# Performance work log

Measured on AMD Instinct MI355X. Metric: run time of the kernel, lower is better.

The kernel has to match this reference:

```python
import jax, jax.numpy as jnp
import numpy as np

EPS = 1e-5

def _ln(x, g=None, b=None):
    m = x.mean(-1, keepdims=True)
    v = x.var(-1, keepdims=True)
    y = (x - m) / jnp.sqrt(v + EPS)
    if g is not None:
        y = y * g + b
    return y

def setup_inputs() -> dict:
    B, N, D, E, NC = 32, 256, 1024, 4096, 16
    key = jax.random.key(0)
    ks = iter(jax.random.split(key, 24))
    def rn(shape, s=0.02):
        return jax.random.normal(next(ks), shape, jnp.float32) * s
    return dict(
        h=jax.random.normal(next(ks), (B, N, D), jnp.float32),
        Wpp=rn((D, E)), bpp=jnp.zeros(E), Wsp=rn((D, E)), bsp=jnp.zeros(E),
        Wq=rn((E, E)), bq=jnp.zeros(E),
        Wk=rn((E, E)), bk=jnp.zeros(E),
        Wv=rn((E, E)), bv=jnp.zeros(E),
        g_pfs=jnp.ones(D + E), b_pfs=jnp.zeros(D + E),
        Wpfs=rn((D + E, D)), bpfs=jnp.zeros(D),
        g_sfs=jnp.ones(E), b_sfs=jnp.zeros(E),
        Wsfs=rn((E, D)), bsfs=jnp.zeros(D),
        Wpc=rn((D, NC)), bpc=jnp.zeros(NC),
        Wc0=rn((NC, 8, D)), bc0=jnp.zeros((NC, 8)),
        Wc1=rn((NC, 16, D)), bc1=jnp.zeros((NC, 16)),
        Wc2=rn((NC, 32, D)), bc2=jnp.zeros((NC, 32)),
    )

def reference(h, Wpp, bpp, Wsp, bsp, Wq, bq, Wk, bk, Wv, bv,
              g_pfs, b_pfs, Wpfs, bpfs, g_sfs, b_sfs, Wsfs, bsfs,
              Wpc, bpc, Wc0, bc0, Wc1, bc1, Wc2, bc2):
    B, N, D = h.shape
    H = 4
    E = Wpp.shape[1]
    hd = E // H
    scale = hd ** -0.5
    gelu = lambda x: jax.nn.gelu(x, approximate=False)  # torch exact GELU
    pp = gelu(h @ Wpp + bpp)                  # [B,N,E]
    sp = gelu(h @ Wsp + bsp)                  # [B,N,E]
    Q = (pp @ Wq + bq).reshape(B, N, H, hd)
    K = (sp @ Wk + bk).reshape(B, N, H, hd)
    V = (sp @ Wv + bv).reshape(B, N, H, hd)
    attn = jax.nn.softmax(jnp.einsum('bqhd,bkhd->bhqk', Q, K) * scale, axis=-1)
    intf = jnp.einsum('bhqk,bkhd->bqhd', attn, V).reshape(B, N, E)
    intf = _ln(intf)                          # F.layer_norm, no affine
    pvec = _ln((_ln(jnp.concatenate([h, intf], -1), g_pfs, b_pfs) @ Wpfs + bpfs).mean(1))  # [B,D]
    svec = _ln((_ln(sp, g_sfs, b_sfs) @ Wsfs + bsfs).mean(1))                               # [B,D]
    parent_logits = pvec @ Wpc + bpc          # [B,NC]
    y_hat = jnp.argmax(parent_logits, axis=1) # argmax(softmax) == argmax(logits)
    # routed child heads: gather per-sample weight by parent argmax, batched matvec
    child = tuple(
        jnp.einsum('bd,bnd->bn', svec, W[y_hat]) + b[y_hat]
        for W, b in ((Wc0, bc0), (Wc1, bc1), (Wc2, bc2))
    )
    return (parent_logits,) + child + (pvec, svec)
```

## Files before the change

### kernel.cpp

```cpp
#include <hip/hip_runtime.h>
#include <hip/hip_bf16.h>

typedef __bf16 bf16x8 __attribute__((ext_vector_type(8)));
typedef float f32x4 __attribute__((ext_vector_type(4)));
typedef unsigned long long u64;

#define EPSV 1e-5f

__device__ __forceinline__ float bf2f(unsigned short u){
  unsigned int x = ((unsigned int)u) << 16;
  return __builtin_bit_cast(float, x);
}
__device__ __forceinline__ unsigned short f2bf(float f){
  __bf16 b = (__bf16)f;
  return __builtin_bit_cast(unsigned short, b);
}
__device__ __forceinline__ float gelu_exact(float x){
  return 0.5f * x * (1.0f + erff(x * 0.7071067811865476f));
}
__device__ __forceinline__ void gload_lds16(const void* g, void* l){
  __builtin_amdgcn_global_load_lds((const __attribute__((address_space(1))) unsigned int*)g,
                                   (__attribute__((address_space(3))) unsigned int*)l, 16, 0, 0);
}

template<int MODE>
__global__ __launch_bounds__(512, 2)
void gemm256(const unsigned short* __restrict__ A, const unsigned short* __restrict__ B,
             const float* __restrict__ bias0, const float* __restrict__ bias1,
             void* __restrict__ C0v, void* __restrict__ C1v,
             int Kd, int lda, int ldb, int ldc)
{
  __shared__ char smem[131072];
  const int t = threadIdx.x;
  const int w = t >> 6, l = t & 63;
  const int wm = w >> 2, wn = w & 3;
  const int lr = l & 15, lg = l >> 4;
  const int nbx = gridDim.x;
  const int nwg = nbx * gridDim.y;
  int bid = blockIdx.y*nbx + blockIdx.x;
  if ((nwg & 7) == 0) bid = (bid & 7)*(nwg >> 3) + (bid >> 3);
  const int bm0 = (bid / nbx) * 256, bn0 = (bid % nbx) * 256;
  const int nk = Kd >> 6;

  const int srow = t >> 3;
  const int sslot = t & 7;

  f32x4 acc[8][4];
  #pragma unroll
  for (int i=0;i<8;++i){
    #pragma unroll
    for (int j=0;j<4;++j){ f32x4 zz = {0.f,0.f,0.f,0.f}; acc[i][j] = zz; }
  }
  bf16x8 a0[4][2], a1[4][2], b0[2][2], b1[2][2];

  auto stage = [&](int kt, int mat, int hf, int q){
    if (kt >= nk) return;
    const int r_h = q*64 + srow;
    const int s_ = sslot ^ ((r_h >> 1) & 7);
    const unsigned short* gp = (mat ? B + (size_t)(bn0 + hf*128 + r_h)*ldb
                                    : A + (size_t)(bm0 + hf*128 + r_h)*lda)
                               + (kt << 6) + s_*8;
    char* lp = smem + mat*65536 + (kt&1)*32768 + hf*16384 + q*8192 + t*16;
    gload_lds16((const void*)gp, (void*)lp);
  };
  auto rdA = [&](int d, int fm, int kk)->bf16x8{
    const int r = fm*16 + lr;
    const int s_ = (kk*4 + lg) ^ ((r >> 1) & 7);
    return *(const bf16x8*)(smem + d*32768 + wm*16384 + r*128 + s_*16);
  };
  auto rdB = [&](int d, int fn, int kk)->bf16x8{
    const int r = (wn&1)*64 + fn*16 + lr;
    const int s_ = (kk*4 + lg) ^ ((r >> 1) & 7);
    return *(const bf16x8*)(smem + 65536 + d*32768 + (wn>>1)*16384 + r*128 + s_*16);
  };

  auto ktile = [&](int kt, int d){
    #pragma unroll
    for (int fm=0; fm<4; ++fm){ a0[fm][0] = rdA(d, fm, 0); a0[fm][1] = rdA(d, fm, 1); }
    #pragma unroll
    for (int fn=0; fn<2; ++fn){ b0[fn][0] = rdB(d, fn, 0); b0[fn][1] = rdB(d, fn, 1); }
    stage(kt+1, 0, 0, 1); stage(kt+1, 0, 1, 1);
    __builtin_amdgcn_s_barrier();
    __builtin_amdgcn_sched_barrier(0);
    __builtin_amdgcn_s_setprio(1);
    #pragma unroll
    for (int fm=0; fm<4; ++fm)
      #pragma unroll
      for (int fn=0; fn<2; ++fn)
        #pragma unroll
        for (int kk=0; kk<2; ++kk)
          acc[fm][fn] = __builtin_amdgcn_mfma_f32_16x16x32_bf16(a0[fm][kk], b0[fn][kk], acc[fm][fn], 0,0,0);
    __builtin_amdgcn_s_setprio(0);
    __builtin_amdgcn_s_barrier();
    #pragma unroll
    for (int fn=0; fn<2; ++fn){ b1[fn][0] = rdB(d, fn+2, 0); b1[fn][1] = rdB(d, fn+2, 1); }
    stage(kt+2, 0, 0, 0); stage(kt+2, 0, 1, 0);
    __builtin_amdgcn_s_barrier();
    __builtin_amdgcn_sched_barrier(0);
    __builtin_amdgcn_s_setprio(1);
    #pragma unroll
    for (int fm=0; fm<4; ++fm)
      #pragma unroll
      for (int fn=0; fn<2; ++fn)
        #pragma unroll
        for (int kk=0; kk<2; ++kk)
          acc[fm][fn+2] = __builtin_amdgcn_mfma_f32_16x16x32_bf16(a0[fm][kk], b1[fn][kk], acc[fm][fn+2], 0,0,0);
    __builtin_amdgcn_s_setprio(0);
    __builtin_amdgcn_s_barrier();
    #pragma unroll
    for (int fm=0; fm<4; ++fm){ a1[fm][0] = rdA(d, fm+4, 0); a1[fm][1] = rdA(d, fm+4, 1); }
    stage(kt+2, 1, 0, 0); stage(kt+2, 1, 1, 0);
    __builtin_amdgcn_s_barrier();
    __builtin_amdgcn_sched_barrier(0);
    __builtin_amdgcn_s_setprio(1);
    #pragma unroll
    for (int fm=0; fm<4; ++fm)
      #pragma unroll
      for (int fn=0; fn<2; ++fn)
        #pragma unroll
        for (int kk=0; kk<2; ++kk)
          acc[fm+4][fn+2] = __builtin_amdgcn_mfma_f32_16x16x32_bf16(a1[fm][kk], b1[fn][kk], acc[fm+4][fn+2], 0,0,0);
    __builtin_amdgcn_s_setprio(0);
    __builtin_amdgcn_s_barrier();
    stage(kt+2, 1, 0, 1); stage(kt+2, 1, 1, 1);
    __builtin_amdgcn_s_setprio(1);
    #pragma unroll
    for (int fm=0; fm<4; ++fm)
      #pragma unroll
      for (int fn=0; fn<2; ++fn)
        #pragma unroll
        for (int kk=0; kk<2; ++kk)
          acc[fm+4][fn] = __builtin_amdgcn_mfma_f32_16x16x32_bf16(a1[fm][kk], b0[fn][kk], acc[fm+4][fn], 0,0,0);
    __builtin_amdgcn_s_setprio(0);
    if (kt + 2 < nk) { asm volatile("s_waitcnt vmcnt(6)" ::: "memory"); }
    else             { asm volatile("s_waitcnt vmcnt(0)" ::: "memory"); }
    __builtin_amdgcn_s_barrier();
  };

  stage(0,0,0,0); stage(0,0,1,0); stage(0,0,0,1); stage(0,0,1,1);
  stage(0,1,0,0); stage(0,1,1,0); stage(0,1,0,1); stage(0,1,1,1);
  stage(1,0,0,0); stage(1,0,1,0);
  stage(1,1,0,0); stage(1,1,1,0); stage(1,1,0,1); stage(1,1,1,1);
  asm volatile("s_waitcnt vmcnt(6)" ::: "memory");
  __builtin_amdgcn_s_barrier();

  for (int kt = 0; kt < nk; kt += 2){ ktile(kt, 0); ktile(kt+1, 1); }

  #pragma unroll
  for (int fm=0; fm<8; ++fm){
    #pragma unroll
    for (int fn=0; fn<4; ++fn){
      const int row0 = bm0 + wm*128 + fm*16 + lg*4;
      const int col  = bn0 + wn*64 + fn*16 + lr;
      f32x4 v = acc[fm][fn];
      if constexpr (MODE == 3){
        unsigned short* C = (unsigned short*)C0v;
        const float bb = bias0[col];
        u64 pack = 0;
        #pragma unroll
        for (int j=0;j<4;++j) pack |= (u64)f2bf(v[j] + bb) << (16*j);
        *(u64*)(C + (size_t)col*256 + (size_t)(row0>>8)*1048576 + (row0&255)) = pack;
      } else if constexpr (MODE == 4){
        if (col < 4096){
          unsigned short* C = (unsigned short*)C0v;
          const float bb = bias0[col];
          #pragma unroll
          for (int j=0;j<4;++j) C[(size_t)(row0+j)*ldc + col] = f2bf(v[j] + bb);
        } else {
          const int c2 = col - 4096;
          unsigned short* C = (unsigned short*)C1v;
          const float bb = bias1[c2];
          u64 pack = 0;
          #pragma unroll
          for (int j=0;j<4;++j) pack |= (u64)f2bf(v[j] + bb) << (16*j);
          *(u64*)(C + (size_t)c2*256 + (size_t)(row0>>8)*1048576 + (row0&255)) = pack;
        }
      } else {
        const bool hi = (MODE == 0) && (col >= 4096);
        unsigned short* C = (unsigned short*)(hi ? C1v : C0v);
        const int c2 = hi ? (col - 4096) : col;
        const float bb = hi ? bias1[c2] : bias0[c2];
        #pragma unroll
        for (int j=0;j<4;++j){
          float x = v[j] + bb;
          if constexpr (MODE==0) x = gelu_exact(x);
          C[(size_t)(row0+j)*ldc + c2] = f2bf(x);
        }
      }
    }
  }
}

template<int MODE>
__global__ __launch_bounds__(256)
void gemm_bt(const unsigned short* __restrict__ A, const unsigned short* __restrict__ B,
             const float* __restrict__ bias, void* __restrict__ Cv,
             int Kd, int lda, int ldb, int ldc,
             long sA2, long sA1, long sB2, long sB1, long sC2, long sC1,
             float scale)
{
  __shared__ unsigned short lds[2][2][4096];
  const int t = threadIdx.x;
  const int w = t >> 6, l = t & 63;
  const int z = blockIdx.z;
  A += (size_t)(z>>2)*sA2 + (size_t)(z&3)*sA1;
  B += (size_t)(z>>2)*sB2 + (size_t)(z&3)*sB1;
  const int bm0 = blockIdx.y * 128, bn0 = blockIdx.x * 128;
  const int nk = Kd >> 5;

  const int sr = l >> 2;
  const int ss = l & 3;

  f32x4 acc[4][4];
  #pragma unroll
  for (int i=0;i<4;++i){
    #pragma unroll
    for (int j=0;j<4;++j){ f32x4 zz = {0.f,0.f,0.f,0.f}; acc[i][j] = zz; }
  }

  const int wm = w >> 1, wn = w & 1;
  const int lr = l & 15, lg = l >> 4;

  auto stage = [&](int kt, int bb){
    const int k0 = kt << 5;
    #pragma unroll
    for (int i=0;i<2;++i){
      const int r  = w*32 + i*16 + sr;
      const int sa = ss ^ ((r>>1)&3);
      const unsigned short* ga = A + (size_t)(bm0 + r)*lda + (k0 + sa*8);
      gload_lds16((const void*)ga, (void*)((char*)&lds[bb][0][0] + w*2048 + i*1024));
      const unsigned short* gb = B + (size_t)(bn0 + r)*ldb + (k0 + sa*8);
      gload_lds16((const void*)gb, (void*)((char*)&lds[bb][1][0] + w*2048 + i*1024));
    }
  };

  int buf = 0;
  stage(0, 0);
  for (int kt=0; kt<nk; ++kt){
    __syncthreads();
    if (kt+1 < nk) stage(kt+1, buf^1);
    bf16x8 av[4], bv[4];
    #pragma unroll
    for (int fm=0; fm<4; ++fm){
      const int row = wm*64 + fm*16 + lr;
      const int sl  = lg ^ ((row>>1)&3);
      av[fm] = *(const bf16x8*)((const char*)&lds[buf][0][0] + row*64 + sl*16);
    }
    #pragma unroll
    for (int fn=0; fn<4; ++fn){
      const int col = wn*64 + fn*16 + lr;
      const int sl  = lg ^ ((col>>1)&3);
      bv[fn] = *(const bf16x8*)((const char*)&lds[buf][1][0] + col*64 + sl*16);
    }
    #pragma unroll
    for (int fm=0; fm<4; ++fm){
      #pragma unroll
      for (int fn=0; fn<4; ++fn)
        acc[fm][fn] = __builtin_amdgcn_mfma_f32_16x16x32_bf16(av[fm], bv[fn], acc[fm][fn], 0,0,0);
    }
    buf ^= 1;
  }

  const size_t coff = (size_t)(z>>2)*sC2 + (size_t)(z&3)*sC1;
  #pragma unroll
  for (int fm=0; fm<4; ++fm){
    #pragma unroll
    for (int fn=0; fn<4; ++fn){
      const int row0 = bm0 + wm*64 + fm*16 + lg*4;
      const int col  = bn0 + wn*64 + fn*16 + lr;
      f32x4 v = acc[fm][fn];
      if constexpr (MODE == 2){
        float* C = (float*)Cv + coff;
        #pragma unroll
        for (int j=0;j<4;++j) C[(size_t)(row0+j)*ldc + col] = v[j]*scale;
      }
    }
  }
}

__global__ __launch_bounds__(256)
void k_convh(const float* __restrict__ in, unsigned short* __restrict__ out){
  const size_t id = (size_t)blockIdx.x*256 + threadIdx.x;
  float4 v = ((const float4*)in)[id];
  u64 pack = (u64)f2bf(v.x) | ((u64)f2bf(v.y)<<16) | ((u64)f2bf(v.z)<<32) | ((u64)f2bf(v.w)<<48);
  *(u64*)(out + id*4) = pack;
}

__global__ __launch_bounds__(256)
void k_tconv(const float* __restrict__ W, unsigned short* __restrict__ Wt, int Kd, int N){
  __shared__ float lt[64][65];
  const int t = threadIdx.x;
  const int n0 = blockIdx.x*64, k0 = blockIdx.y*64;
  #pragma unroll
  for (int i=0;i<16;++i){
    int lin = i*256 + t; int r = lin>>6, c = lin&63;
    lt[r][c] = W[(size_t)(k0+r)*N + n0 + c];
  }
  __syncthreads();
  #pragma unroll
  for (int i=0;i<16;++i){
    int lin = i*256 + t; int n = lin>>6, k = lin&63;
    Wt[(size_t)(n0+n)*Kd + k0 + k] = f2bf(lt[k][n]);
  }
}

__global__ __launch_bounds__(256)
void k_softmax(const float* __restrict__ S, unsigned short* __restrict__ P){
  const int t = threadIdx.x, w = t>>6, l = t&63;
  const size_t row = (size_t)blockIdx.x*4 + w;
  float4 v = *(const float4*)(S + row*256 + l*4);
  float m = fmaxf(fmaxf(v.x,v.y), fmaxf(v.z,v.w));
  #pragma unroll
  for (int off=32; off; off>>=1) m = fmaxf(m, __shfl_xor(m, off));
  float e0 = expf(v.x-m), e1 = expf(v.y-m), e2 = expf(v.z-m), e3 = expf(v.w-m);
  float s = e0+e1+e2+e3;
  #pragma unroll
  for (int off=32; off; off>>=1) s += __shfl_xor(s, off);
  const float inv = 1.0f/s;
  u64 pack = (u64)f2bf(e0*inv) | ((u64)f2bf(e1*inv)<<16) | ((u64)f2bf(e2*inv)<<32) | ((u64)f2bf(e3*inv)<<48);
  *(u64*)(P + row*256 + l*4) = pack;
}

__device__ __forceinline__ void blkred2(float& a, float& b, float* sred, int t){
  #pragma unroll
  for (int off=32; off; off>>=1){ a += __shfl_xor(a, off); b += __shfl_xor(b, off); }
  __syncthreads();
  if ((t&63)==0){ sred[(t>>6)*2] = a; sred[(t>>6)*2+1] = b; }
  __syncthreads();
  a = sred[0]+sred[2]+sred[4]+sred[6];
  b = sred[1]+sred[3]+sred[5]+sred[7];
}

__global__ __launch_bounds__(256)
void k_stats(const float* __restrict__ h, const float* __restrict__ intf,
             const unsigned short* __restrict__ sp,
             const float* __restrict__ g_pfs, const float* __restrict__ b_pfs,
             const float* __restrict__ g_sfs, const float* __restrict__ b_sfs,
             float* __restrict__ part_p, float* __restrict__ part_s, int g0)
{
  __shared__ float sred[8];
  const int bl = blockIdx.x, grp = blockIdx.y, t = threadIdx.x;
  float zacc[20], wacc[16];
  #pragma unroll
  for (int j=0;j<20;++j) zacc[j]=0.f;
  #pragma unroll
  for (int j=0;j<16;++j) wacc[j]=0.f;
  for (int rr=0; rr<32; ++rr){
    const size_t r = (size_t)bl*256 + grp*32 + rr;
    float hv[4], iv[16], sv[16];
    #pragma unroll
    for (int j=0;j<4;++j) hv[j] = h[r*1024 + j*256 + t];
    float s1=0.f, s2=0.f;
    #pragma unroll
    for (int j=0;j<16;++j){ float x = intf[r*4096 + j*256 + t]; iv[j]=x; s1+=x; s2+=x*x; }
    blkred2(s1,s2,sred,t);
    const float m1 = s1*(1.f/4096.f);
    const float rs1 = rsqrtf(fmaxf(s2*(1.f/4096.f) - m1*m1, 0.f) + EPSV);
    float t1=0.f, t2=0.f;
    #pragma unroll
    for (int j=0;j<4;++j){ t1 += hv[j]; t2 += hv[j]*hv[j]; }
    #pragma unroll
    for (int j=0;j<16;++j){ float y = (iv[j]-m1)*rs1; iv[j]=y; t1+=y; t2+=y*y; }
    blkred2(t1,t2,sred,t);
    const float m2 = t1*(1.f/5120.f);
    const float rs2 = rsqrtf(fmaxf(t2*(1.f/5120.f) - m2*m2, 0.f) + EPSV);
    #pragma unroll
    for (int j=0;j<4;++j){ int idx = j*256+t; zacc[j] += ((hv[j]-m2)*rs2)*g_pfs[idx] + b_pfs[idx]; }
    #pragma unroll
    for (int j=0;j<16;++j){ int idx = 1024 + j*256+t; zacc[4+j] += ((iv[j]-m2)*rs2)*g_pfs[idx] + b_pfs[idx]; }
    float u1=0.f, u2=0.f;
    #pragma unroll
    for (int j=0;j<16;++j){ float x = bf2f(sp[r*4096 + j*256 + t]); sv[j]=x; u1+=x; u2+=x*x; }
    blkred2(u1,u2,sred,t);
    const float m3 = u1*(1.f/4096.f);
    const float rs3 = rsqrtf(fmaxf(u2*(1.f/4096.f) - m3*m3, 0.f) + EPSV);
    #pragma unroll
    for (int j=0;j<16;++j){ int idx = j*256+t; wacc[j] += ((sv[j]-m3)*rs3)*g_sfs[idx] + b_sfs[idx]; }
  }
  const size_t pb = (size_t)(g0 + bl)*8 + grp;
  #pragma unroll
  for (int j=0;j<20;++j) part_p[pb*5120 + j*256 + t] = zacc[j];
  #pragma unroll
  for (int j=0;j<16;++j) part_s[pb*4096 + j*256 + t] = wacc[j];
}

__global__ __launch_bounds__(256)
void k_reduce(const float* __restrict__ part_p, const float* __restrict__ part_s,
              float* __restrict__ xbar, float* __restrict__ ybar){
  int id = blockIdx.x*256 + threadIdx.x;
  if (id < 32*5120){
    const int b = id / 5120, i = id % 5120;
    float s = 0.f;
    for (int g=0; g<8; ++g) s += part_p[((size_t)b*8+g)*5120 + i];
    xbar[(size_t)b*5120 + i] = s * (1.f/256.f);
  } else {
    id -= 32*5120;
    const int b = id / 4096, i = id % 4096;
    float s = 0.f;
    for (int g=0; g<8; ++g) s += part_s[((size_t)b*8+g)*4096 + i];
    ybar[(size_t)b*4096 + i] = s * (1.f/256.f);
  }
}

__global__ __launch_bounds__(256)
void k_proj_part(const float* __restrict__ xbar, const float* __restrict__ ybar,
                 const float* __restrict__ Wpfs, const float* __restrict__ Wsfs,
                 float* __restrict__ pbuf){
  const int path = blockIdx.z;
  const int y = blockIdx.y;
  if (path == 1 && y >= 8) return;
  const int Kp = path ? 4096 : 5120;
  const float* X = path ? ybar : xbar;
  const float* W = path ? Wsfs : Wpfs;
  const int t = threadIdx.x;
  const int col = blockIdx.x*64 + (t & 63);
  const int sub = t >> 6;
  const int k0 = y*512 + sub*128;
  float acc[32];
  #pragma unroll
  for (int b=0;b<32;++b) acc[b] = 0.f;
  for (int i4=0; i4<32; ++i4){
    const int k = k0 + i4*4;
    float wv0 = W[(size_t)(k  )*1024 + col];
    float wv1 = W[(size_t)(k+1)*1024 + col];
    float wv2 = W[(size_t)(k+2)*1024 + col];
    float wv3 = W[(size_t)(k+3)*1024 + col];
    #pragma unroll
    for (int b=0;b<32;++b){
      float4 xv = *(const float4*)(X + (size_t)b*Kp + k);
      acc[b] += xv.x*wv0 + xv.y*wv1 + xv.z*wv2 + xv.w*wv3;
    }
  }
  float* dst = pbuf + ((size_t)(path*40 + y*4 + sub)*32)*1024 + col;
  #pragma unroll
  for (int b=0;b<32;++b) dst[(size_t)b*1024] = acc[b];
}

__global__ __launch_bounds__(256)
void k_projred(const float* __restrict__ pbuf,
               const float* __restrict__ bpfs, const float* __restrict__ bsfs,
               float* __restrict__ tpre, float* __restrict__ spre){
  const int id = blockIdx.x*256 + threadIdx.x;
  const int path = id >> 15;
  const int rem = id & 32767;
  const int b = rem >> 10, col = rem & 1023;
  const int ns = path ? 32 : 40;
  const float* src = pbuf + ((size_t)(path*40)*32 + b)*1024 + col;
  float s = path ? bsfs[col] : bpfs[col];
  for (int g=0; g<ns; ++g) s += src[(size_t)g*32*1024];
  (path ? spre : tpre)[(size_t)b*1024 + col] = s;
}

__global__ __launch_bounds__(256)
void k_lnrow(const float* __restrict__ tpre, const float* __restrict__ spre,
             float* __restrict__ out){
  __shared__ float sred[8];
  const int id = blockIdx.x, t = threadIdx.x;
  const int path = id >> 5, b = id & 31;
  const float* src = (path ? spre : tpre) + (size_t)b*1024;
  float v[4]; float s1=0.f, s2=0.f;
  #pragma unroll
  for (int j=0;j<4;++j){ v[j] = src[j*256+t]; s1 += v[j]; s2 += v[j]*v[j]; }
  blkred2(s1,s2,sred,t);
  const float m = s1*(1.f/1024.f);
  const float rs = rsqrtf(fmaxf(s2*(1.f/1024.f)-m*m,0.f)+EPSV);
  float* dst = out + (path ? 35072 : 2304) + (size_t)b*1024;
  #pragma unroll
  for (int j=0;j<4;++j) dst[j*256+t] = (v[j]-m)*rs;
}

__global__ __launch_bounds__(256)
void k_head(const float* __restrict__ Wpc, const float* __restrict__ bpc,
            const float* __restrict__ Wc0, const float* __restrict__ bc0,
            const float* __restrict__ Wc1, const float* __restrict__ bc1,
            const float* __restrict__ Wc2, const float* __restrict__ bc2,
            float* __restrict__ out){
  __shared__ float slog[16];
  __shared__ int sy;
  const int b = blockIdx.x, t = threadIdx.x, w = t>>6, l = t&63;
  const float* pv = out + 2304 + (size_t)b*1024;
  const float* sv = out + 35072 + (size_t)b*1024;
  #pragma unroll
  for (int jj=0; jj<4; ++jj){
    const int j = w*4 + jj;
    float a = 0.f;
    for (int i=l; i<1024; i+=64) a += pv[i]*Wpc[(size_t)i*16 + j];
    #pragma unroll
    for (int off=32; off; off>>=1) a += __shfl_xor(a, off);
    if (l==0){ const float lgv = a + bpc[j]; slog[j] = lgv; out[b*16 + j] = lgv; }
  }
  __syncthreads();
  if (t==0){
    int best=0; float bvv = slog[0];
    for (int i=1;i<16;++i) if (slog[i] > bvv){ bvv = slog[i]; best = i; }
    sy = best;
  }
  __syncthreads();
  const int y = sy;
  const float* Ws[3] = {Wc0, Wc1, Wc2};
  const float* bs[3] = {bc0, bc1, bc2};
  const int nouts[3] = {8,16,32};
  const int ooff[3]  = {512, 768, 1280};
  for (int hI=0; hI<3; ++hI){
    const int no = nouts[hI];
    for (int n = w; n < no; n += 4){
      const float* wr = Ws[hI] + ((size_t)y*no + n)*1024;
      float a = 0.f;
      for (int i=l; i<1024; i+=64) a += sv[i]*wr[i];
      #pragma unroll
      for (int off=32; off; off>>=1) a += __shfl_xor(a, off);
      if (l==0) out[ooff[hI] + b*no + n] = a + bs[hI][(size_t)y*no + n];
    }
  }
}

extern "C" void kernel_launch(void* const* d_in, const int* in_sizes, int n_in,
                              void* d_out, int out_size, void* d_ws, size_t ws_size,
                              hipStream_t stream)
{
  const float* h    = (const float*)d_in[0];
  const float* Wpp  = (const float*)d_in[1];
  const float* bpp  = (const float*)d_in[2];
  const float* Wsp  = (const float*)d_in[3];
  const float* bsp  = (const float*)d_in[4];
  const float* Wq   = (const float*)d_in[5];
  const float* bq   = (const float*)d_in[6];
  const float* Wk   = (const float*)d_in[7];
  const float* bk   = (const float*)d_in[8];
  const float* Wv   = (const float*)d_in[9];
  const float* bv   = (const float*)d_in[10];
  const float* g_pfs= (const float*)d_in[11];
  const float* b_pfs= (const float*)d_in[12];
  const float* Wpfs = (const float*)d_in[13];
  const float* bpfs = (const float*)d_in[14];
  const float* g_sfs= (const float*)d_in[15];
  const float* b_sfs= (const float*)d_in[16];
  const float* Wsfs = (const float*)d_in[17];
  const float* bsfs = (const float*)d_in[18];
  const float* Wpc  = (const float*)d_in[19];
  const float* bpc  = (const float*)d_in[20];
  const float* Wc0  = (const float*)d_in[21];
  const float* bc0  = (const float*)d_in[22];
  const float* Wc1  = (const float*)d_in[23];
  const float* bc1  = (const float*)d_in[24];
  const float* Wc2  = (const float*)d_in[25];
  const float* bc2  = (const float*)d_in[26];
  float* out = (float*)d_out;
  char* ws = (char*)d_ws;
  (void)in_sizes; (void)n_in; (void)out_size;

  struct PlanT { int G, NS, hoist; };
  const PlanT plans[11] = {
    {32,4096,1},{32,4096,0},{16,4096,1},{16,4096,0},{8,4096,1},{8,4096,0},
    {4,4096,0},{2,4096,0},{1,4096,0},{1,2048,0},{1,1024,0}};
  int G = 0, NS = 0, HOIST = 0;
  size_t oWt=0,oWps=0,oWq=0,oWkv=0;
  size_t oPp=0,oPs=0,oXb=0,oYb=0,oTp=0,oSp=0,oPbf=0,oHb=0,oPb=0,oSb=0,oQ=0,oK=0,oVt=0,oS=0,oP=0;
  for (int pi = 0; pi < 11; ++pi){
    const size_t g = plans[pi].G, ns = plans[pi].NS;
    const int hoist = plans[pi].hoist;
    size_t off = 0;
    auto alloc = [&](size_t bytes){ size_t o = off; off += (bytes + 255) & ~255ULL; return o; };
    size_t wt=0, wps=0, wq=0, wkv=0;
    if (hoist){
      wps = alloc(8192ULL*1024*2);
      wq  = alloc(4096ULL*4096*2);
      wkv = alloc(8192ULL*4096*2);
    } else {
      wt = alloc(ns*4096*2);
    }
    size_t pp_ = alloc(32*8*5120*4);
    size_t ps_ = alloc(32*8*4096*4);
    size_t xb = alloc(32*5120*4);
    size_t yb = alloc(32*4096*4);
    size_t tp = alloc(32*1024*4);
    size_t sp_ = alloc(32*1024*4);
    size_t pbf = alloc(2*40*32*1024*4);
    size_t hb = alloc(g*524288);
    size_t pb = alloc(g*2097152);
    size_t sb = alloc(g*2097152);
    size_t q  = alloc(g*2097152);
    size_t k  = alloc(g*2097152);
    size_t vt = alloc(g*2097152);
    size_t s  = alloc(g*1048576);
    size_t p  = alloc(g*524288);
    if (off <= ws_size){
      G = (int)g; NS = (int)ns; HOIST = hoist;
      oWt=wt; oWps=wps; oWq=wq; oWkv=wkv;
      oPp=pp_; oPs=ps_; oXb=xb; oYb=yb; oTp=tp; oSp=sp_; oPbf=pbf;
      oHb=hb; oPb=pb; oSb=sb; oQ=q; oK=k; oVt=vt; oS=s; oP=p;
      break;
    }
  }
  if (!G) return;

  unsigned short* Wt   = (unsigned short*)(ws + oWt);
  unsigned short* WpsT = (unsigned short*)(ws + oWps);
  unsigned short* WqT  = (unsigned short*)(ws + oWq);
  unsigned short* WkvT = (unsigned short*)(ws + oWkv);
  float* part_p = (float*)(ws + oPp);
  float* part_s = (float*)(ws + oPs);
  float* xbar   = (float*)(ws + oXb);
  float* ybar   = (float*)(ws + oYb);
  float* tpre   = (float*)(ws + oTp);
  float* spre   = (float*)(ws + oSp);
  float* pbuf   = (float*)(ws + oPbf);
  unsigned short* h_bf = (unsigned short*)(ws + oHb);
  unsigned short* pp   = (unsigned short*)(ws + oPb);
  unsigned short* sp   = (unsigned short*)(ws + oSb);
  unsigned short* Q    = (unsigned short*)(ws + oQ);
  unsigned short* Kb   = (unsigned short*)(ws + oK);
  unsigned short* Vt   = (unsigned short*)(ws + oVt);
  float*          S    = (float*)(ws + oS);
  unsigned short* P    = (unsigned short*)(ws + oP);
  float*          intf = (float*)(ws + oQ);

  const float scale = 1.0f/32.0f;
  (void)oK;

  if (HOIST){
    hipLaunchKernelGGL(k_tconv, dim3(64,16), dim3(256), 0, stream, Wpp, WpsT, 1024, 4096);
    hipLaunchKernelGGL(k_tconv, dim3(64,16), dim3(256), 0, stream, Wsp, WpsT + 4096ULL*1024, 1024, 4096);
    hipLaunchKernelGGL(k_tconv, dim3(64,64), dim3(256), 0, stream, Wq, WqT, 4096, 4096);
    hipLaunchKernelGGL(k_tconv, dim3(64,64), dim3(256), 0, stream, Wk, WkvT, 4096, 4096);
    hipLaunchKernelGGL(k_tconv, dim3(64,64), dim3(256), 0, stream, Wv, WkvT + 4096ULL*4096, 4096, 4096);
  }

  for (int g0 = 0; g0 < 32; g0 += G){
    const float* h_g = h + (size_t)g0*262144;

    hipLaunchKernelGGL(k_convh, dim3(G*256), dim3(256), 0, stream, h_g, h_bf);

    if (HOIST){
      hipLaunchKernelGGL(gemm256<0>, dim3(32,G), dim3(512), 0, stream,
                         h_bf, WpsT, bpp, bsp, (void*)pp, (void*)sp, 1024, 1024,1024,4096);
      hipLaunchKernelGGL(gemm256<1>, dim3(16,G), dim3(512), 0, stream,
                         pp, WqT, bq, bq, (void*)Q, (void*)Q, 4096, 4096,4096,4096);
      hipLaunchKernelGGL(gemm256<4>, dim3(32,G), dim3(512), 0, stream,
                         sp, WkvT, bk, bv, (void*)Kb, (void*)Vt, 4096, 4096,4096,4096);
    } else {
      hipLaunchKernelGGL(k_tconv, dim3(64,16), dim3(256), 0, stream, Wpp, Wt, 1024, 4096);
      hipLaunchKernelGGL(gemm256<0>, dim3(16,G), dim3(512), 0, stream,
                         h_bf, Wt, bpp, bpp, (void*)pp, (void*)pp, 1024, 1024,1024,4096);
      for (int nso = 0; nso < 4096; nso += NS){
        hipLaunchKernelGGL(k_tconv, dim3(NS/64,64), dim3(256), 0, stream, Wq + nso, Wt, 4096, 4096);
        hipLaunchKernelGGL(gemm256<1>, dim3(NS/256,G), dim3(512), 0, stream,
                           pp, Wt, bq + nso, bq + nso, (void*)(Q + nso), (void*)(Q + nso), 4096, 4096,4096,4096);
      }
      hipLaunchKernelGGL(k_tconv, dim3(64,16), dim3(256), 0, stream, Wsp, Wt, 1024, 4096);
      hipLaunchKernelGGL(gemm256<0>, dim3(16,G), dim3(512), 0, stream,
                         h_bf, Wt, bsp, bsp, (void*)sp, (void*)sp, 1024, 1024,1024,4096);
      for (int nso = 0; nso < 4096; nso += NS){
        hipLaunchKernelGGL(k_tconv, dim3(NS/64,64), dim3(256), 0, stream, Wk + nso, Wt, 4096, 4096);
        hipLaunchKernelGGL(gemm256<1>, dim3(NS/256,G), dim3(512), 0, stream,
                           sp, Wt, bk + nso, bk + nso, (void*)(Kb + nso), (void*)(Kb + nso), 4096, 4096,4096,4096);
      }
      for (int nso = 0; nso < 4096; nso += NS){
        hipLaunchKernelGGL(k_tconv, dim3(NS/64,64), dim3(256), 0, stream, Wv + nso, Wt, 4096, 4096);
        hipLaunchKernelGGL(gemm256<3>, dim3(NS/256,G), dim3(512), 0, stream,
                           sp, Wt, bv + nso, bv + nso, (void*)(Vt + (size_t)nso*256), (void*)(Vt + (size_t)nso*256), 4096, 4096,4096,256);
      }
    }
    hipLaunchKernelGGL(gemm_bt<2>, dim3(2,2,G*4), dim3(256), 0, stream,
                       Q, Kb, (const float*)nullptr, (void*)S, 1024, 4096,4096,256,
                       1048576L,1024L, 1048576L,1024L, 262144L,65536L, scale);
    hipLaunchKernelGGL(k_softmax, dim3(G*256), dim3(256), 0, stream, S, P);
    hipLaunchKernelGGL(gemm_bt<2>, dim3(8,2,G*4), dim3(256), 0, stream,
                       P, Vt, (const float*)nullptr, (void*)intf, 256, 256,256,4096,
                       262144L,65536L, 1048576L,262144L, 1048576L,1024L, 1.f);
    hipLaunchKernelGGL(k_stats, dim3(G,8), dim3(256), 0, stream,
                       h_g, intf, sp, g_pfs, b_pfs, g_sfs, b_sfs, part_p, part_s, g0);
  }

  hipLaunchKernelGGL(k_reduce, dim3(1152), dim3(256), 0, stream, part_p, part_s, xbar, ybar);
  hipLaunchKernelGGL(k_proj_part, dim3(16,10,2), dim3(256), 0, stream,
                     xbar, ybar, Wpfs, Wsfs, pbuf);
  hipLaunchKernelGGL(k_projred, dim3(256), dim3(256), 0, stream,
                     pbuf, bpfs, bsfs, tpre, spre);
  hipLaunchKernelGGL(k_lnrow, dim3(64), dim3(256), 0, stream, tpre, spre, out);
  hipLaunchKernelGGL(k_head, dim3(32), dim3(256), 0, stream,
                     Wpc, bpc, Wc0, bc0, Wc1, bc1, Wc2, bc2, out);
}
```

Before: 1.518 ms.

## Restructure GEMM k-tile pipeline to prefetch next-tile fragments and finer vmcnt gating

Reorders the four MFMA quadrants per k-tile and moves loading of the a0/b0 register fragments for the next k-tile into the current tile, so the first quadrant of each tile starts without waiting on LDS reads. The staging of global-to-LDS copies is reshuffled and each phase now waits on a vmcnt(4) gate instead of a single vmcnt(6)/0 at the end. The sched_barrier hints are removed. This aims to overlap LDS reads and global loads with MFMA work more evenly. The new vmcnt accounting and staging order must still line up with the buffer reuse, or the kernel can read stale LDS data.

```diff
diff --git a/kernel.cpp b/kernel.cpp
--- a/kernel.cpp
+++ b/kernel.cpp
@@ -22,6 +22,8 @@
   __builtin_amdgcn_global_load_lds((const __attribute__((address_space(1))) unsigned int*)g,
                                    (__attribute__((address_space(3))) unsigned int*)l, 16, 0, 0);
 }
+
+#define VMGATE4() asm volatile("s_waitcnt vmcnt(4)" ::: "memory")
 
 template<int MODE>
 __global__ __launch_bounds__(512, 2)
@@ -76,12 +78,9 @@
 
   auto ktile = [&](int kt, int d){
     #pragma unroll
-    for (int fm=0; fm<4; ++fm){ a0[fm][0] = rdA(d, fm, 0); a0[fm][1] = rdA(d, fm, 1); }
-    #pragma unroll
-    for (int fn=0; fn<2; ++fn){ b0[fn][0] = rdB(d, fn, 0); b0[fn][1] = rdB(d, fn, 1); }
-    stage(kt+1, 0, 0, 1); stage(kt+1, 0, 1, 1);
-    __builtin_amdgcn_s_barrier();
-    __builtin_amdgcn_sched_barrier(0);
+    for (int fm=0; fm<4; ++fm){ a1[fm][0] = rdA(d, fm+4, 0); a1[fm][1] = rdA(d, fm+4, 1); }
+    stage(kt+1, 1, 0, 1); stage(kt+1, 1, 1, 1);
+    __builtin_amdgcn_s_barrier();
     __builtin_amdgcn_s_setprio(1);
     #pragma unroll
     for (int fm=0; fm<4; ++fm)
@@ -91,12 +90,25 @@
         for (int kk=0; kk<2; ++kk)
           acc[fm][fn] = __builtin_amdgcn_mfma_f32_16x16x32_bf16(a0[fm][kk], b0[fn][kk], acc[fm][fn], 0,0,0);
     __builtin_amdgcn_s_setprio(0);
+    VMGATE4();
     __builtin_amdgcn_s_barrier();
     #pragma unroll
     for (int fn=0; fn<2; ++fn){ b1[fn][0] = rdB(d, fn+2, 0); b1[fn][1] = rdB(d, fn+2, 1); }
+    stage(kt+1, 0, 0, 1); stage(kt+1, 0, 1, 1);
+    __builtin_amdgcn_s_barrier();
+    __builtin_amdgcn_s_setprio(1);
+    #pragma unroll
+    for (int fm=0; fm<4; ++fm)
+      #pragma unroll
+      for (int fn=0; fn<2; ++fn)
+        #pragma unroll
+        for (int kk=0; kk<2; ++kk)
+          acc[fm+4][fn] = __builtin_amdgcn_mfma_f32_16x16x32_bf16(a1[fm][kk], b0[fn][kk], acc[fm+4][fn], 0,0,0);
+    __builtin_amdgcn_s_setprio(0);
+    VMGATE4();
+    __builtin_amdgcn_s_barrier();
     stage(kt+2, 0, 0, 0); stage(kt+2, 0, 1, 0);
     __builtin_amdgcn_s_barrier();
-    __builtin_amdgcn_sched_barrier(0);
     __builtin_amdgcn_s_setprio(1);
     #pragma unroll
     for (int fm=0; fm<4; ++fm)
@@ -106,12 +118,16 @@
         for (int kk=0; kk<2; ++kk)
           acc[fm][fn+2] = __builtin_amdgcn_mfma_f32_16x16x32_bf16(a0[fm][kk], b1[fn][kk], acc[fm][fn+2], 0,0,0);
     __builtin_amdgcn_s_setprio(0);
-    __builtin_amdgcn_s_barrier();
-    #pragma unroll
-    for (int fm=0; fm<4; ++fm){ a1[fm][0] = rdA(d, fm+4, 0); a1[fm][1] = rdA(d, fm+4, 1); }
+    VMGATE4();
+    __builtin_amdgcn_s_barrier();
+    if (kt+1 < nk){
+      #pragma unroll
+      for (int fm=0; fm<4; ++fm){ a0[fm][0] = rdA(d^1, fm, 0); a0[fm][1] = rdA(d^1, fm, 1); }
+      #pragma unroll
+      for (int fn=0; fn<2; ++fn){ b0[fn][0] = rdB(d^1, fn, 0); b0[fn][1] = rdB(d^1, fn, 1); }
+    }
     stage(kt+2, 1, 0, 0); stage(kt+2, 1, 1, 0);
     __builtin_amdgcn_s_barrier();
-    __builtin_amdgcn_sched_barrier(0);
     __builtin_amdgcn_s_setprio(1);
     #pragma unroll
     for (int fm=0; fm<4; ++fm)
@@ -121,27 +137,23 @@
         for (int kk=0; kk<2; ++kk)
           acc[fm+4][fn+2] = __builtin_amdgcn_mfma_f32_16x16x32_bf16(a1[fm][kk], b1[fn][kk], acc[fm+4][fn+2], 0,0,0);
     __builtin_amdgcn_s_setprio(0);
-    __builtin_amdgcn_s_barrier();
-    stage(kt+2, 1, 0, 1); stage(kt+2, 1, 1, 1);
-    __builtin_amdgcn_s_setprio(1);
-    #pragma unroll
-    for (int fm=0; fm<4; ++fm)
-      #pragma unroll
-      for (int fn=0; fn<2; ++fn)
-        #pragma unroll
-        for (int kk=0; kk<2; ++kk)
-          acc[fm+4][fn] = __builtin_amdgcn_mfma_f32_16x16x32_bf16(a1[fm][kk], b0[fn][kk], acc[fm+4][fn], 0,0,0);
-    __builtin_amdgcn_s_setprio(0);
-    if (kt + 2 < nk) { asm volatile("s_waitcnt vmcnt(6)" ::: "memory"); }
-    else             { asm volatile("s_waitcnt vmcnt(0)" ::: "memory"); }
+    VMGATE4();
     __builtin_amdgcn_s_barrier();
   };
 
-  stage(0,0,0,0); stage(0,0,1,0); stage(0,0,0,1); stage(0,0,1,1);
-  stage(0,1,0,0); stage(0,1,1,0); stage(0,1,0,1); stage(0,1,1,1);
+  stage(0,0,0,0); stage(0,0,1,0);
+  stage(0,1,0,0); stage(0,1,1,0);
+  stage(0,1,0,1); stage(0,1,1,1);
+  stage(0,0,0,1); stage(0,0,1,1);
   stage(1,0,0,0); stage(1,0,1,0);
-  stage(1,1,0,0); stage(1,1,1,0); stage(1,1,0,1); stage(1,1,1,1);
+  stage(1,1,0,0); stage(1,1,1,0);
   asm volatile("s_waitcnt vmcnt(6)" ::: "memory");
+  __builtin_amdgcn_s_barrier();
+  #pragma unroll
+  for (int fm=0; fm<4; ++fm){ a0[fm][0] = rdA(0, fm, 0); a0[fm][1] = rdA(0, fm, 1); }
+  #pragma unroll
+  for (int fn=0; fn<2; ++fn){ b0[fn][0] = rdB(0, fn, 0); b0[fn][1] = rdB(0, fn, 1); }
+  VMGATE4();
   __builtin_amdgcn_s_barrier();
 
   for (int kt = 0; kt < nk; kt += 2){ ktile(kt, 0); ktile(kt+1, 1); }
```

Measured after the change: 1.784 ms. 1.17x slower.

## Alias attention scratch onto projection buffers and add shared transposed-weight mode

Applied to the files above, without the earlier changes.

Drops the separate S and P scratch buffers and places them inside the pp buffer region, which is dead by the time attention scores are computed. This shrinks the workspace footprint, so larger batch groups with hoisted weights can fit. A new middle mode keeps one large shared transposed-weight buffer and runs fused pp/sp and K/V GEMMs per group, re-transposing weights each group. The plan list also no longer tries G=32, which caps the group size at 16 and may add launches if G=32 previously fit.

```diff
diff --git a/kernel.cpp b/kernel.cpp
--- a/kernel.cpp
+++ b/kernel.cpp
@@ -549,23 +549,25 @@
   char* ws = (char*)d_ws;
   (void)in_sizes; (void)n_in; (void)out_size;
 
-  struct PlanT { int G, NS, hoist; };
-  const PlanT plans[11] = {
-    {32,4096,1},{32,4096,0},{16,4096,1},{16,4096,0},{8,4096,1},{8,4096,0},
-    {4,4096,0},{2,4096,0},{1,4096,0},{1,2048,0},{1,1024,0}};
-  int G = 0, NS = 0, HOIST = 0;
+  struct PlanT { int G, NS, mode; };
+  const PlanT plans[12] = {
+    {16,4096,2},{16,4096,1},{16,4096,0},{8,4096,2},{8,4096,1},{8,4096,0},
+    {4,4096,0},{2,4096,0},{1,4096,0},{1,4096,0},{1,2048,0},{1,1024,0}};
+  int G = 0, NS = 0, MODE_ = 0;
   size_t oWt=0,oWps=0,oWq=0,oWkv=0;
-  size_t oPp=0,oPs=0,oXb=0,oYb=0,oTp=0,oSp=0,oPbf=0,oHb=0,oPb=0,oSb=0,oQ=0,oK=0,oVt=0,oS=0,oP=0;
-  for (int pi = 0; pi < 11; ++pi){
+  size_t oPp=0,oPs=0,oXb=0,oYb=0,oTp=0,oSp=0,oPbf=0,oHb=0,oPb=0,oSb=0,oQ=0,oK=0,oVt=0;
+  for (int pi = 0; pi < 12; ++pi){
     const size_t g = plans[pi].G, ns = plans[pi].NS;
-    const int hoist = plans[pi].hoist;
+    const int mode = plans[pi].mode;
     size_t off = 0;
     auto alloc = [&](size_t bytes){ size_t o = off; off += (bytes + 255) & ~255ULL; return o; };
     size_t wt=0, wps=0, wq=0, wkv=0;
-    if (hoist){
+    if (mode == 2){
       wps = alloc(8192ULL*1024*2);
       wq  = alloc(4096ULL*4096*2);
       wkv = alloc(8192ULL*4096*2);
+    } else if (mode == 1){
+      wt = alloc(8192ULL*4096*2);
     } else {
       wt = alloc(ns*4096*2);
     }
@@ -582,13 +584,11 @@
     size_t q  = alloc(g*2097152);
     size_t k  = alloc(g*2097152);
     size_t vt = alloc(g*2097152);
-    size_t s  = alloc(g*1048576);
-    size_t p  = alloc(g*524288);
     if (off <= ws_size){
-      G = (int)g; NS = (int)ns; HOIST = hoist;
+      G = (int)g; NS = (int)ns; MODE_ = mode;
       oWt=wt; oWps=wps; oWq=wq; oWkv=wkv;
       oPp=pp_; oPs=ps_; oXb=xb; oYb=yb; oTp=tp; oSp=sp_; oPbf=pbf;
-      oHb=hb; oPb=pb; oSb=sb; oQ=q; oK=k; oVt=vt; oS=s; oP=p;
+      oHb=hb; oPb=pb; oSb=sb; oQ=q; oK=k; oVt=vt;
       break;
     }
   }
@@ -611,14 +611,14 @@
   unsigned short* Q    = (unsigned short*)(ws + oQ);
   unsigned short* Kb   = (unsigned short*)(ws + oK);
   unsigned short* Vt   = (unsigned short*)(ws + oVt);
-  float*          S    = (float*)(ws + oS);
-  unsigned short* P    = (unsigned short*)(ws + oP);
+  float*          S    = (float*)(ws + oPb);
+  unsigned short* P    = (unsigned short*)(ws + oPb + (size_t)G*1048576);
   float*          intf = (float*)(ws + oQ);
 
   const float scale = 1.0f/32.0f;
   (void)oK;
 
-  if (HOIST){
+  if (MODE_ == 2){
     hipLaunchKernelGGL(k_tconv, dim3(64,16), dim3(256), 0, stream, Wpp, WpsT, 1024, 4096);
     hipLaunchKernelGGL(k_tconv, dim3(64,16), dim3(256), 0, stream, Wsp, WpsT + 4096ULL*1024, 1024, 4096);
     hipLaunchKernelGGL(k_tconv, dim3(64,64), dim3(256), 0, stream, Wq, WqT, 4096, 4096);
@@ -631,13 +631,25 @@
 
     hipLaunchKernelGGL(k_convh, dim3(G*256), dim3(256), 0, stream, h_g, h_bf);
 
-    if (HOIST){
+    if (MODE_ == 2){
       hipLaunchKernelGGL(gemm256<0>, dim3(32,G), dim3(512), 0, stream,
                          h_bf, WpsT, bpp, bsp, (void*)pp, (void*)sp, 1024, 1024,1024,4096);
       hipLaunchKernelGGL(gemm256<1>, dim3(16,G), dim3(512), 0, stream,
                          pp, WqT, bq, bq, (void*)Q, (void*)Q, 4096, 4096,4096,4096);
       hipLaunchKernelGGL(gemm256<4>, dim3(32,G), dim3(512), 0, stream,
                          sp, WkvT, bk, bv, (void*)Kb, (void*)Vt, 4096, 4096,4096,4096);
+    } else if (MODE_ == 1){
+      hipLaunchKernelGGL(k_tconv, dim3(64,16), dim3(256), 0, stream, Wpp, Wt, 1024, 4096);
+      hipLaunchKernelGGL(k_tconv, dim3(64,16), dim3(256), 0, stream, Wsp, Wt + 4096ULL*1024, 1024, 4096);
+      hipLaunchKernelGGL(gemm256<0>, dim3(32,G), dim3(512), 0, stream,
+                         h_bf, Wt, bpp, bsp, (void*)pp, (void*)sp, 1024, 1024,1024,4096);
+      hipLaunchKernelGGL(k_tconv, dim3(64,64), dim3(256), 0, stream, Wq, Wt, 4096, 4096);
+      hipLaunchKernelGGL(gemm256<1>, dim3(16,G), dim3(512), 0, stream,
+                         pp, Wt, bq, bq, (void*)Q, (void*)Q, 4096, 4096,4096,4096);
+      hipLaunchKernelGGL(k_tconv, dim3(64,64), dim3(256), 0, stream, Wk, Wt, 4096, 4096);
+      hipLaunchKernelGGL(k_tconv, dim3(64,64), dim3(256), 0, stream, Wv, Wt + 4096ULL*4096, 4096, 4096);
+      hipLaunchKernelGGL(gemm256<4>, dim3(32,G), dim3(512), 0, stream,
+                         sp, Wt, bk, bv, (void*)Kb, (void*)Vt, 4096, 4096,4096,4096);
     } else {
       hipLaunchKernelGGL(k_tconv, dim3(64,16), dim3(256), 0, stream, Wpp, Wt, 1024, 4096);
       hipLaunchKernelGGL(gemm256<0>, dim3(16,G), dim3(512), 0, stream,
```

New measurement: 1.538 ms. No clear change (+1.3%).
